# Kernel optimization log

Measured on AMD Instinct MI355X. Metric: run time of the kernel, lower is better.

The kernel has to match this reference:

```python
import jax, jax.numpy as jnp
from jax import lax
import numpy as np

BN_EPS = 1e-5  # nn.BatchNorm2d default eps (eval mode with running stats)


def setup_inputs() -> dict:
    key = jax.random.key(0)
    ks = jax.random.split(key, 6)
    B, C, O, H, W = 4, 64, 64, 128, 128
    x = jax.random.normal(ks[0], (B, C, H, W), jnp.float32)
    # conv_offset: 27 = 3 * deform_groups * kh * kw output channels, zero-bias.
    # Scaled small to mimic the near-zero init of ModulatedDeformConv2dPack.
    w_off = jax.random.normal(ks[1], (27, C, 3, 3), jnp.float32) * 0.05
    b_off = jnp.zeros((27,), jnp.float32)
    weight = jax.random.normal(ks[2], (O, C, 3, 3), jnp.float32) * (1.0 / np.sqrt(C * 9))
    bias = jax.random.normal(ks[3], (O,), jnp.float32) * 0.1
    gamma = jax.random.normal(ks[4], (O,), jnp.float32) * 0.1 + 1.0
    beta = jax.random.normal(ks[5], (O,), jnp.float32) * 0.1
    running_mean = jnp.zeros((O,), jnp.float32)
    running_var = jnp.ones((O,), jnp.float32)
    return {"x": x, "w_off": w_off, "b_off": b_off, "weight": weight, "bias": bias,
            "gamma": gamma, "beta": beta, "running_mean": running_mean, "running_var": running_var}


def _dcn_bn_relu(x, w_off, b_off, weight, bias, gamma, beta, running_mean, running_var):
    B, C, H, W = x.shape
    O = weight.shape[0]
    K = 9  # 3x3 kernel taps
    # --- offset/mask conv (regular 3x3, stride 1, pad 1) ---
    off = lax.conv_general_dilated(x, w_off, (1, 1), ((1, 1), (1, 1)),
                                   dimension_numbers=("NCHW", "OIHW", "NCHW"))
    off = off + b_off[None, :, None, None]
    o1, o2, m = jnp.split(off, 3, axis=1)  # each [B,9,H,W]
    # mmcv layout: cat(o1,o2) then interpreted as (tap, [y,x]) pairs
    offset = jnp.concatenate([o1, o2], axis=1).reshape(B, K, 2, H, W)
    mask = jax.nn.sigmoid(m)  # [B,K,H,W]
    # --- sampling grid: p = (h - pad + i*dil + dy, w - pad + j*dil + dx) ---
    ky = (jnp.repeat(jnp.arange(3), 3) - 1).astype(x.dtype)  # [K]
    kx = (jnp.tile(jnp.arange(3), 3) - 1).astype(x.dtype)
    py = jnp.arange(H, dtype=x.dtype)[None, None, :, None] + ky[None, :, None, None] + offset[:, :, 0]
    px = jnp.arange(W, dtype=x.dtype)[None, None, None, :] + kx[None, :, None, None] + offset[:, :, 1]
    y0 = jnp.floor(py); x0 = jnp.floor(px)
    dy = py - y0; dx = px - x0  # [B,K,H,W]
    y0i = y0.astype(jnp.int32); x0i = x0.astype(jnp.int32)

    def gather(yi, xi):
        # zero outside bounds (mmcv bilinear semantics)
        valid = (yi >= 0) & (yi < H) & (xi >= 0) & (xi < W)
        yc = jnp.clip(yi, 0, H - 1)
        xc = jnp.clip(xi, 0, W - 1)
        g = jax.vmap(lambda xb, yb, xb2: xb[:, yb, xb2])(x, yc, xc)  # [B,C,K,H,W]
        return g * valid[:, None].astype(x.dtype)

    w00 = ((1 - dy) * (1 - dx))[:, None]
    w01 = ((1 - dy) * dx)[:, None]
    w10 = (dy * (1 - dx))[:, None]
    w11 = (dy * dx)[:, None]
    samp = (gather(y0i, x0i) * w00 + gather(y0i, x0i + 1) * w01 +
            gather(y0i + 1, x0i) * w10 + gather(y0i + 1, x0i + 1) * w11)
    samp = samp * mask[:, None]  # modulation, [B,C,K,H,W]
    # conv accumulation over (channel, tap)
    out = jnp.einsum("ock,bckhw->bohw", weight.reshape(O, C, K), samp)
    out = out + bias[None, :, None, None]
    # --- BatchNorm2d (eval, running stats) + ReLU ---
    scale = gamma / jnp.sqrt(running_var + BN_EPS)
    out = (out - running_mean[None, :, None, None]) * scale[None, :, None, None] + beta[None, :, None, None]
    return jax.nn.relu(out)


def reference(x, w_off, b_off, weight, bias, gamma, beta, running_mean, running_var):
    return _dcn_bn_relu(x, w_off, b_off, weight, bias, gamma, beta, running_mean, running_var)
```

## Files before the change

### kernel.cpp

```cpp
#include <hip/hip_runtime.h>
#include <hip/hip_bf16.h>


#define HH 128
#define WW 128
#define KP2 200

typedef __attribute__((ext_vector_type(8))) short bf16x8;
typedef __attribute__((ext_vector_type(4))) float f32x4;

__device__ __forceinline__ unsigned short f2bf(float f) {
    union { __hip_bfloat16 b; unsigned short u; } cv;
    cv.b = __float2bfloat16(f);
    return cv.u;
}
__device__ __forceinline__ float bf2f(unsigned short u) {
    union { unsigned int i; float f; } cv;
    cv.i = ((unsigned int)u) << 16;
    return cv.f;
}

#define WBM_ELEMS 36864
#define WBO_ELEMS 18432
#define XT_OFF    55296

__global__ __launch_bounds__(256) void transpose_kernel(
    const float* __restrict__ x,
    const float* __restrict__ w_off,
    const float* __restrict__ wgt,
    unsigned short* __restrict__ ws)
{
    __shared__ float tile[64 * 65];
    const int tid = threadIdx.x;

    {
        int t = blockIdx.x * 256 + tid;
        if (t < WBM_ELEMS) {
            int j = t & 7, lane = (t >> 3) & 63, nt = (t >> 9) & 3, kb = t >> 11;
            int k = kb * 32 + ((lane >> 4) << 3) + j;
            int n = nt * 16 + (lane & 15);
            int tap = k >> 6, c = k & 63;
            ws[t] = f2bf(wgt[n * 576 + c * 9 + tap]);
        } else if (t < WBM_ELEMS + WBO_ELEMS) {
            int t2 = t - WBM_ELEMS;
            int j = t2 & 7, lane = (t2 >> 3) & 63, nt = (t2 >> 9) & 1, kb = t2 >> 10;
            int k = kb * 32 + ((lane >> 4) << 3) + j;
            int n = nt * 16 + (lane & 15);
            int tap = k >> 6, c = k & 63;
            ws[t] = (n < 27) ? f2bf(w_off[n * 576 + c * 9 + tap]) : (unsigned short)0;
        }
    }

    const int bb  = blockIdx.x >> 8;
    const int hw0 = (blockIdx.x & 255) << 6;
    const float* xb = x + ((size_t)bb << 20);
#pragma unroll
    for (int it = 0; it < 16; ++it) {
        int idx = it * 256 + tid;
        int c = idx >> 6, i = idx & 63;
        tile[c * 65 + i] = xb[(c << 14) + hw0 + i];
    }
    __syncthreads();
    unsigned int* xtb = (unsigned int*)(ws + XT_OFF) + ((size_t)bb << 19);
#pragma unroll
    for (int it = 0; it < 8; ++it) {
        int idx = it * 256 + tid;
        int i = idx >> 5, c2 = idx & 31;
        unsigned int lo = (unsigned int)f2bf(tile[(2 * c2) * 65 + i]);
        unsigned int hi = (unsigned int)f2bf(tile[(2 * c2 + 1) * 65 + i]);
        xtb[(size_t)(hw0 + i) * 32 + c2] = lo | (hi << 16);
    }
}

__global__ __launch_bounds__(128) void DeformConv_14568529068723_kernel(
    const float* __restrict__ b_off,
    const float* __restrict__ bias,
    const float* __restrict__ gamma,
    const float* __restrict__ beta,
    const float* __restrict__ rmean,
    const float* __restrict__ rvar,
    const unsigned short* __restrict__ ws,
    float* __restrict__ out)
{
    __shared__ __align__(16) unsigned short samp[32 * KP2];
    __shared__ float eL[4][9][32];
    __shared__ int   oL[2][9][32];
    __shared__ float sbuf[176];

    const int tid  = threadIdx.x;
    const int wv   = tid >> 6;
    const int lane = tid & 63;
    const int px16 = lane & 15;
    const int cg   = lane >> 4;
    const int c8   = tid & 7;
    const int pxq  = tid >> 3;

    if (tid < 64) {
        float sc = gamma[tid] * __frsqrt_rn(rvar[tid] + 1e-5f);
        sbuf[tid] = sc;
        sbuf[64 + tid] = (bias[tid] - rmean[tid]) * sc + beta[tid];
        if (tid < 27) sbuf[128 + tid] = b_off[tid];
    }

    const int bid = blockIdx.x;
    const int swz = ((bid & 7) << 8) + (bid >> 3);
    const int p0   = swz * 32;
    const int b    = p0 >> 14;
    const int rem0 = p0 & 16383;
    const int h    = rem0 >> 7;
    const int w0   = rem0 & 127;
    const unsigned short* xt = ws + XT_OFF + ((size_t)b << 20);

    const bf16x8* WbM = (const bf16x8*)ws;
    const bf16x8* WbO = (const bf16x8*)(ws + WBM_ELEMS);

    __syncthreads();

    f32x4 accO[2];
#pragma unroll
    for (int q = 0; q < 2; ++q) accO[q] = (f32x4){0.f, 0.f, 0.f, 0.f};

    for (int chk = 0; chk < 3; ++chk) {
#pragma unroll
        for (int tl = 0; tl < 3; ++tl) {
            int tap = chk * 3 + tl;
            int ky = tap / 3 - 1, kx = tap % 3 - 1;
            int yy = h + ky;
            int yc = min(max(yy, 0), HH - 1);
            bool oky = (yy >= 0) & (yy < HH);
#pragma unroll
            for (int it = 0; it < 2; ++it) {
                int px = it * 16 + pxq;
                int xx = w0 + px + kx;
                bool ok = oky & (xx >= 0) & (xx < WW);
                int pos = yc * WW + min(max(xx, 0), WW - 1);
                uint4 v = *(const uint4*)(xt + pos * 64 + (c8 << 3));
                if (!ok) { v.x = 0u; v.y = 0u; v.z = 0u; v.w = 0u; }
                *(uint4*)&samp[px * KP2 + tl * 64 + (c8 << 3)] = v;
            }
        }
        __syncthreads();
#pragma unroll
        for (int st = 0; st < 6; ++st) {
            int kb = chk * 6 + st;
            bf16x8 b0 = WbO[(kb * 2 + 0) * 64 + lane];
            bf16x8 b1 = WbO[(kb * 2 + 1) * 64 + lane];
            bf16x8 af = *(const bf16x8*)&samp[(wv * 16 + px16) * KP2 + st * 32 + (cg << 3)];
            accO[0] = __builtin_amdgcn_mfma_f32_16x16x32_bf16(af, b0, accO[0], 0, 0, 0);
            accO[1] = __builtin_amdgcn_mfma_f32_16x16x32_bf16(af, b1, accO[1], 0, 0, 0);
        }
        __syncthreads();
    }
    float* offs = (float*)samp;
    {
        int n0 = lane & 15;
        int mB = cg * 4;
#pragma unroll
        for (int r = 0; r < 4; ++r) {
            int pxc = wv * 16 + mB + r;
            offs[n0 * 32 + pxc] = accO[0][r] + sbuf[128 + n0];
            int n1 = 16 + n0;
            if (n1 < 27) {
                float vv = accO[1][r] + sbuf[128 + n1];
                if (n1 >= 18) vv = 1.0f / (1.0f + __expf(-vv));
                offs[n1 * 32 + pxc] = vv;
            }
        }
    }
    __syncthreads();

#pragma unroll
    for (int base = 0; base < 288; base += 128) {
        int idx = base + tid;
        if (idx < 288) {
            int px = idx & 31, tap = idx >> 5;
            float o1 = offs[(2 * tap) * 32 + px];
            float o2 = offs[(2 * tap + 1) * 32 + px];
            float m  = offs[(18 + tap) * 32 + px];
            float py  = (float)(h + tap / 3 - 1) + o1;
            float pxf = (float)(w0 + px + tap % 3 - 1) + o2;
            float y0f = floorf(py), x0f = floorf(pxf);
            float dy = py - y0f, dx = pxf - x0f;
            int y0 = (int)y0f, x0 = (int)x0f;
            int y1 = y0 + 1, x1 = x0 + 1;
            int yc0 = min(max(y0, 0), HH - 1), yc1 = min(max(y1, 0), HH - 1);
            int xc0 = min(max(x0, 0), WW - 1), xc1 = min(max(x1, 0), WW - 1);
            float vy0 = (y0 >= 0 && y0 < HH) ? 1.0f : 0.0f;
            float vy1 = (y1 >= 0 && y1 < HH) ? 1.0f : 0.0f;
            float vx0 = (x0 >= 0 && x0 < WW) ? 1.0f : 0.0f;
            float vx1 = (x1 >= 0 && x1 < WW) ? 1.0f : 0.0f;
            float c00 = (1.0f - dy) * (1.0f - dx) * m * vy0 * vx0;
            float c01 = (1.0f - dy) * dx * m * vy0 * vx1;
            float c10 = dy * (1.0f - dx) * m * vy1 * vx0;
            float c11 = dy * dx * m * vy1 * vx1;
            int bx = min(xc0, WW - 2);
            bool s0 = (xc0 != bx), s1 = (xc1 != bx);
            eL[0][tap][px] = (s0 ? 0.f : c00) + (s1 ? 0.f : c01);
            eL[1][tap][px] = (s0 ? c00 : 0.f) + (s1 ? c01 : 0.f);
            eL[2][tap][px] = (s0 ? 0.f : c10) + (s1 ? 0.f : c11);
            eL[3][tap][px] = (s0 ? c10 : 0.f) + (s1 ? c11 : 0.f);
            oL[0][tap][px] = (yc0 * WW + bx) * 64;
            oL[1][tap][px] = (yc1 * WW + bx) * 64;
        }
    }
    __syncthreads();

    f32x4 acc[4];
#pragma unroll
    for (int nt = 0; nt < 4; ++nt) acc[nt] = (f32x4){0.f, 0.f, 0.f, 0.f};

    for (int chk = 0; chk < 3; ++chk) {
#pragma unroll
        for (int tl = 0; tl < 3; ++tl) {
            int tap = chk * 3 + tl;
#pragma unroll
            for (int it = 0; it < 2; ++it) {
                int px = it * 16 + pxq;
                int o0 = oL[0][tap][px], o1r = oL[1][tap][px];
                float e0 = eL[0][tap][px], e1 = eL[1][tap][px];
                float e2 = eL[2][tap][px], e3 = eL[3][tap][px];
                uint4 a0 = *(const uint4*)(xt + o0 + (c8 << 3));
                uint4 a1 = *(const uint4*)(xt + o0 + 64 + (c8 << 3));
                uint4 b0 = *(const uint4*)(xt + o1r + (c8 << 3));
                uint4 b1 = *(const uint4*)(xt + o1r + 64 + (c8 << 3));
                const unsigned int* pa0 = (const unsigned int*)&a0;
                const unsigned int* pa1 = (const unsigned int*)&a1;
                const unsigned int* pb0 = (const unsigned int*)&b0;
                const unsigned int* pb1 = (const unsigned int*)&b1;
                uint4 pk;
                unsigned int* pp = (unsigned int*)&pk;
#pragma unroll
                for (int q = 0; q < 4; ++q) {
                    float lo = e0 * bf2f((unsigned short)(pa0[q] & 0xffff))
                             + e1 * bf2f((unsigned short)(pa1[q] & 0xffff))
                             + e2 * bf2f((unsigned short)(pb0[q] & 0xffff))
                             + e3 * bf2f((unsigned short)(pb1[q] & 0xffff));
                    float hi = e0 * bf2f((unsigned short)(pa0[q] >> 16))
                             + e1 * bf2f((unsigned short)(pa1[q] >> 16))
                             + e2 * bf2f((unsigned short)(pb0[q] >> 16))
                             + e3 * bf2f((unsigned short)(pb1[q] >> 16));
                    pp[q] = (unsigned int)f2bf(lo) | ((unsigned int)f2bf(hi) << 16);
                }
                *(uint4*)&samp[px * KP2 + tl * 64 + (c8 << 3)] = pk;
            }
        }
        __syncthreads();
#pragma unroll
        for (int st = 0; st < 6; ++st) {
            int kb = chk * 6 + st;
            bf16x8 af = *(const bf16x8*)&samp[(wv * 16 + px16) * KP2 + st * 32 + (cg << 3)];
#pragma unroll
            for (int nt = 0; nt < 4; ++nt) {
                bf16x8 bf = WbM[(kb * 4 + nt) * 64 + lane];
                acc[nt] = __builtin_amdgcn_mfma_f32_16x16x32_bf16(af, bf, acc[nt], 0, 0, 0);
            }
        }
        __syncthreads();
    }

    float* dT = (float*)samp;
    {
        int n0 = lane & 15;
        int mB = cg * 4;
#pragma unroll
        for (int nt = 0; nt < 4; ++nt)
#pragma unroll
            for (int r = 0; r < 4; ++r)
                dT[(nt * 16 + n0) * 33 + wv * 16 + mB + r] = acc[nt][r];
    }
    __syncthreads();
    {
        int px = tid & 31;
        int oh = tid >> 5;
#pragma unroll
        for (int i = 0; i < 16; ++i) {
            int o = 4 * i + oh;
            float v = dT[o * 33 + px];
            v = fmaxf(fmaf(v, sbuf[o], sbuf[64 + o]), 0.0f);
            out[(((size_t)(b * 64 + o)) << 14) + rem0 + px] = v;
        }
    }
}

extern "C" void kernel_launch(void* const* d_in, const int* in_sizes, int n_in,
                              void* d_out, int out_size, void* d_ws, size_t ws_size,
                              hipStream_t stream) {
    (void)in_sizes; (void)n_in; (void)ws_size; (void)out_size;
    const float* x     = (const float*)d_in[0];
    const float* w_off = (const float*)d_in[1];
    const float* b_off = (const float*)d_in[2];
    const float* wgt   = (const float*)d_in[3];
    const float* bias  = (const float*)d_in[4];
    const float* gamma = (const float*)d_in[5];
    const float* beta  = (const float*)d_in[6];
    const float* rmean = (const float*)d_in[7];
    const float* rvar  = (const float*)d_in[8];
    unsigned short* wsB = (unsigned short*)d_ws;
    float* outp = (float*)d_out;

    transpose_kernel<<<dim3(1024), dim3(256), 0, stream>>>(x, w_off, wgt, wsB);
    DeformConv_14568529068723_kernel<<<dim3(2048), dim3(128), 0, stream>>>(
        b_off, bias, gamma, beta, rmean, rvar, wsB, outp);
}
```

Baseline: 119.5 us.

## Double block size to 256 threads and repartition MFMA work across four waves

```diff
diff --git a/kernel.cpp b/kernel.cpp
--- a/kernel.cpp
+++ b/kernel.cpp
@@ -72,7 +72,7 @@
     }
 }
 
-__global__ __launch_bounds__(128) void DeformConv_14568529068723_kernel(
+__global__ __launch_bounds__(256) void DeformConv_14568529068723_kernel(
     const float* __restrict__ b_off,
     const float* __restrict__ bias,
     const float* __restrict__ gamma,
@@ -116,9 +116,9 @@
 
     __syncthreads();
 
-    f32x4 accO[2];
-#pragma unroll
-    for (int q = 0; q < 2; ++q) accO[q] = (f32x4){0.f, 0.f, 0.f, 0.f};
+    const int mtO = wv >> 1;
+    const int ocO = wv & 1;
+    f32x4 accO = (f32x4){0.f, 0.f, 0.f, 0.f};
 
     for (int chk = 0; chk < 3; ++chk) {
 #pragma unroll
@@ -128,49 +128,41 @@
             int yy = h + ky;
             int yc = min(max(yy, 0), HH - 1);
             bool oky = (yy >= 0) & (yy < HH);
-#pragma unroll
-            for (int it = 0; it < 2; ++it) {
-                int px = it * 16 + pxq;
-                int xx = w0 + px + kx;
-                bool ok = oky & (xx >= 0) & (xx < WW);
-                int pos = yc * WW + min(max(xx, 0), WW - 1);
-                uint4 v = *(const uint4*)(xt + pos * 64 + (c8 << 3));
-                if (!ok) { v.x = 0u; v.y = 0u; v.z = 0u; v.w = 0u; }
-                *(uint4*)&samp[px * KP2 + tl * 64 + (c8 << 3)] = v;
-            }
+            int xx = w0 + pxq + kx;
+            bool ok = oky & (xx >= 0) & (xx < WW);
+            int pos = yc * WW + min(max(xx, 0), WW - 1);
+            uint4 v = *(const uint4*)(xt + pos * 64 + (c8 << 3));
+            if (!ok) { v.x = 0u; v.y = 0u; v.z = 0u; v.w = 0u; }
+            *(uint4*)&samp[pxq * KP2 + tl * 64 + (c8 << 3)] = v;
         }
         __syncthreads();
 #pragma unroll
         for (int st = 0; st < 6; ++st) {
             int kb = chk * 6 + st;
-            bf16x8 b0 = WbO[(kb * 2 + 0) * 64 + lane];
-            bf16x8 b1 = WbO[(kb * 2 + 1) * 64 + lane];
-            bf16x8 af = *(const bf16x8*)&samp[(wv * 16 + px16) * KP2 + st * 32 + (cg << 3)];
-            accO[0] = __builtin_amdgcn_mfma_f32_16x16x32_bf16(af, b0, accO[0], 0, 0, 0);
-            accO[1] = __builtin_amdgcn_mfma_f32_16x16x32_bf16(af, b1, accO[1], 0, 0, 0);
+            bf16x8 bO = WbO[(kb * 2 + ocO) * 64 + lane];
+            bf16x8 af = *(const bf16x8*)&samp[(mtO * 16 + px16) * KP2 + st * 32 + (cg << 3)];
+            accO = __builtin_amdgcn_mfma_f32_16x16x32_bf16(af, bO, accO, 0, 0, 0);
         }
         __syncthreads();
     }
     float* offs = (float*)samp;
     {
-        int n0 = lane & 15;
+        int n0 = ocO * 16 + (lane & 15);
         int mB = cg * 4;
 #pragma unroll
         for (int r = 0; r < 4; ++r) {
-            int pxc = wv * 16 + mB + r;
-            offs[n0 * 32 + pxc] = accO[0][r] + sbuf[128 + n0];
-            int n1 = 16 + n0;
-            if (n1 < 27) {
-                float vv = accO[1][r] + sbuf[128 + n1];
-                if (n1 >= 18) vv = 1.0f / (1.0f + __expf(-vv));
-                offs[n1 * 32 + pxc] = vv;
+            int pxc = mtO * 16 + mB + r;
+            if (n0 < 27) {
+                float vv = accO[r] + sbuf[128 + n0];
+                if (n0 >= 18) vv = 1.0f / (1.0f + __expf(-vv));
+                offs[n0 * 32 + pxc] = vv;
             }
         }
     }
     __syncthreads();
 
 #pragma unroll
-    for (int base = 0; base < 288; base += 128) {
+    for (int base = 0; base < 288; base += 256) {
         int idx = base + tid;
         if (idx < 288) {
             int px = idx & 31, tap = idx >> 5;
@@ -205,55 +197,50 @@
     }
     __syncthreads();
 
-    f32x4 acc[4];
-#pragma unroll
-    for (int nt = 0; nt < 4; ++nt) acc[nt] = (f32x4){0.f, 0.f, 0.f, 0.f};
+    f32x4 acc[2];
+#pragma unroll
+    for (int mt = 0; mt < 2; ++mt) acc[mt] = (f32x4){0.f, 0.f, 0.f, 0.f};
 
     for (int chk = 0; chk < 3; ++chk) {
 #pragma unroll
         for (int tl = 0; tl < 3; ++tl) {
             int tap = chk * 3 + tl;
-#pragma unroll
-            for (int it = 0; it < 2; ++it) {
-                int px = it * 16 + pxq;
-                int o0 = oL[0][tap][px], o1r = oL[1][tap][px];
-                float e0 = eL[0][tap][px], e1 = eL[1][tap][px];
-                float e2 = eL[2][tap][px], e3 = eL[3][tap][px];
-                uint4 a0 = *(const uint4*)(xt + o0 + (c8 << 3));
-                uint4 a1 = *(const uint4*)(xt + o0 + 64 + (c8 << 3));
-                uint4 b0 = *(const uint4*)(xt + o1r + (c8 << 3));
-                uint4 b1 = *(const uint4*)(xt + o1r + 64 + (c8 << 3));
-                const unsigned int* pa0 = (const unsigned int*)&a0;
-                const unsigned int* pa1 = (const unsigned int*)&a1;
-                const unsigned int* pb0 = (const unsigned int*)&b0;
-                const unsigned int* pb1 = (const unsigned int*)&b1;
-                uint4 pk;
-                unsigned int* pp = (unsigned int*)&pk;
-#pragma unroll
-                for (int q = 0; q < 4; ++q) {
-                    float lo = e0 * bf2f((unsigned short)(pa0[q] & 0xffff))
-                             + e1 * bf2f((unsigned short)(pa1[q] & 0xffff))
-                             + e2 * bf2f((unsigned short)(pb0[q] & 0xffff))
-                             + e3 * bf2f((unsigned short)(pb1[q] & 0xffff));
-                    float hi = e0 * bf2f((unsigned short)(pa0[q] >> 16))
-                             + e1 * bf2f((unsigned short)(pa1[q] >> 16))
-                             + e2 * bf2f((unsigned short)(pb0[q] >> 16))
-                             + e3 * bf2f((unsigned short)(pb1[q] >> 16));
-                    pp[q] = (unsigned int)f2bf(lo) | ((unsigned int)f2bf(hi) << 16);
-                }
-                *(uint4*)&samp[px * KP2 + tl * 64 + (c8 << 3)] = pk;
+            int o0 = oL[0][tap][pxq], o1r = oL[1][tap][pxq];
+            float e0 = eL[0][tap][pxq], e1 = eL[1][tap][pxq];
+            float e2 = eL[2][tap][pxq], e3 = eL[3][tap][pxq];
+            uint4 a0 = *(const uint4*)(xt + o0 + (c8 << 3));
+            uint4 a1 = *(const uint4*)(xt + o0 + 64 + (c8 << 3));
+            uint4 b0 = *(const uint4*)(xt + o1r + (c8 << 3));
+            uint4 b1 = *(const uint4*)(xt + o1r + 64 + (c8 << 3));
+            const unsigned int* pa0 = (const unsigned int*)&a0;
+            const unsigned int* pa1 = (const unsigned int*)&a1;
+            const unsigned int* pb0 = (const unsigned int*)&b0;
+            const unsigned int* pb1 = (const unsigned int*)&b1;
+            uint4 pk;
+            unsigned int* pp = (unsigned int*)&pk;
+#pragma unroll
+            for (int q = 0; q < 4; ++q) {
+                float lo = e0 * bf2f((unsigned short)(pa0[q] & 0xffff))
+                         + e1 * bf2f((unsigned short)(pa1[q] & 0xffff))
+                         + e2 * bf2f((unsigned short)(pb0[q] & 0xffff))
+                         + e3 * bf2f((unsigned short)(pb1[q] & 0xffff));
+                float hi = e0 * bf2f((unsigned short)(pa0[q] >> 16))
+                         + e1 * bf2f((unsigned short)(pa1[q] >> 16))
+                         + e2 * bf2f((unsigned short)(pb0[q] >> 16))
+                         + e3 * bf2f((unsigned short)(pb1[q] >> 16));
+                pp[q] = (unsigned int)f2bf(lo) | ((unsigned int)f2bf(hi) << 16);
             }
+            *(uint4*)&samp[pxq * KP2 + tl * 64 + (c8 << 3)] = pk;
         }
         __syncthreads();
 #pragma unroll
         for (int st = 0; st < 6; ++st) {
             int kb = chk * 6 + st;
-            bf16x8 af = *(const bf16x8*)&samp[(wv * 16 + px16) * KP2 + st * 32 + (cg << 3)];
-#pragma unroll
-            for (int nt = 0; nt < 4; ++nt) {
-                bf16x8 bf = WbM[(kb * 4 + nt) * 64 + lane];
-                acc[nt] = __builtin_amdgcn_mfma_f32_16x16x32_bf16(af, bf, acc[nt], 0, 0, 0);
-            }
+            bf16x8 bf = WbM[(kb * 4 + wv) * 64 + lane];
+            bf16x8 af0 = *(const bf16x8*)&samp[px16 * KP2 + st * 32 + (cg << 3)];
+            bf16x8 af1 = *(const bf16x8*)&samp[(16 + px16) * KP2 + st * 32 + (cg << 3)];
+            acc[0] = __builtin_amdgcn_mfma_f32_16x16x32_bf16(af0, bf, acc[0], 0, 0, 0);
+            acc[1] = __builtin_amdgcn_mfma_f32_16x16x32_bf16(af1, bf, acc[1], 0, 0, 0);
         }
         __syncthreads();
     }
@@ -263,18 +250,18 @@
         int n0 = lane & 15;
         int mB = cg * 4;
 #pragma unroll
-        for (int nt = 0; nt < 4; ++nt)
+        for (int mt = 0; mt < 2; ++mt)
 #pragma unroll
             for (int r = 0; r < 4; ++r)
-                dT[(nt * 16 + n0) * 33 + wv * 16 + mB + r] = acc[nt][r];
+                dT[(wv * 16 + n0) * 33 + mt * 16 + mB + r] = acc[mt][r];
     }
     __syncthreads();
     {
         int px = tid & 31;
         int oh = tid >> 5;
 #pragma unroll
-        for (int i = 0; i < 16; ++i) {
-            int o = 4 * i + oh;
+        for (int i = 0; i < 8; ++i) {
+            int o = 8 * i + oh;
             float v = dT[o * 33 + px];
             v = fmaxf(fmaf(v, sbuf[o], sbuf[64 + o]), 0.0f);
             out[(((size_t)(b * 64 + o)) << 14) + rem0 + px] = v;
@@ -299,6 +286,6 @@
     float* outp = (float*)d_out;
 
     transpose_kernel<<<dim3(1024), dim3(256), 0, stream>>>(x, w_off, wgt, wsB);
-    DeformConv_14568529068723_kernel<<<dim3(2048), dim3(128), 0, stream>>>(
+    DeformConv_14568529068723_kernel<<<dim3(2048), dim3(256), 0, stream>>>(
         b_off, bias, gamma, beta, rmean, rvar, wsB, outp);
 }
```

Result: faster. 113.3 us (-5.2%).
